# Kernel optimization log

Hardware: AMD Instinct MI355X
Metric: run time of the kernel (lower is better)

Reference implementation:

```python
import jax, jax.numpy as jnp
import numpy as np

DIM = 1024
HEADS = 16
HEAD_DIM = 64
WINDOW = 64


def setup_inputs() -> dict:
    key = jax.random.key(0)
    ks = jax.random.split(key, 9)
    s = lambda fan_in: 1.0 / np.sqrt(fan_in)
    x = jax.random.normal(ks[0], (2, 2048, DIM), dtype=jnp.float32)
    # KANEXLayer: phi = Linear(dim, hidden=dim) -> SiLU -> Linear(dim, dim); g = Linear(dim, 3*H*D)
    W1 = jax.random.uniform(ks[1], (DIM, DIM), jnp.float32, -s(DIM), s(DIM))
    b1 = jax.random.uniform(ks[2], (DIM,), jnp.float32, -s(DIM), s(DIM))
    W2 = jax.random.uniform(ks[3], (DIM, DIM), jnp.float32, -s(DIM), s(DIM))
    b2 = jax.random.uniform(ks[4], (DIM,), jnp.float32, -s(DIM), s(DIM))
    Wg = jax.random.uniform(ks[5], (3 * HEADS * HEAD_DIM, DIM), jnp.float32, -s(DIM), s(DIM))
    bg = jax.random.uniform(ks[6], (3 * HEADS * HEAD_DIM,), jnp.float32, -s(DIM), s(DIM))
    Wo = jax.random.uniform(ks[7], (DIM, HEADS * HEAD_DIM), jnp.float32, -s(HEADS * HEAD_DIM), s(HEADS * HEAD_DIM))
    bo = jax.random.uniform(ks[8], (DIM,), jnp.float32, -s(HEADS * HEAD_DIM), s(HEADS * HEAD_DIM))
    return {"x": x, "W1": W1, "b1": b1, "W2": W2, "b2": b2,
            "Wg": Wg, "bg": bg, "Wo": Wo, "bo": bo}


def reference(x, W1, b1, W2, b2, Wg, bg, Wo, bo):
    b, n, _ = x.shape
    # KANEXLayer: g(phi(x))
    h = jax.nn.silu(x @ W1.T + b1) @ W2.T + b2          # [b, n, dim]
    qkv = h @ Wg.T + bg                                  # [b, n, 3*H*D]
    q, k, v = jnp.split(qkv, 3, axis=-1)
    reshape = lambda t: t.reshape(b, n, HEADS, HEAD_DIM).transpose(0, 2, 1, 3)  # [b, H, n, D]
    q, k, v = reshape(q), reshape(k), reshape(v)
    dots = jnp.einsum('bhid,bhjd->bhij', q, k) * (HEAD_DIM ** -0.5)  # [b, H, n, n]
    # mask positions j >= i + window (triu with diagonal=window_size)
    i = jnp.arange(n)[:, None]
    j = jnp.arange(n)[None, :]
    mask = j >= i + WINDOW                               # [n, n] bool
    dots = jnp.where(mask, -jnp.inf, dots)
    attn = jax.nn.softmax(dots, axis=-1)
    out = jnp.einsum('bhij,bhjd->bhid', attn, v)         # [b, H, n, D]
    out = out.transpose(0, 2, 1, 3).reshape(b, n, HEADS * HEAD_DIM)
    return out @ Wo.T + bo                               # [b, n, dim]
```

## Files before the change

kernel.cpp:

```cpp
#include <hip/hip_runtime.h>

typedef unsigned short u16;
typedef unsigned int   u32;
typedef __bf16 bf16x8 __attribute__((ext_vector_type(8)));
typedef float  f32x4  __attribute__((ext_vector_type(4)));

__device__ __forceinline__ u16 f2bf(float f) {
    return __builtin_bit_cast(u16, (__bf16)f);
}

__device__ __forceinline__ void gload16(const void* g, void* lds) {
    __builtin_amdgcn_global_load_lds(
        (const __attribute__((address_space(1))) u32*)g,
        (__attribute__((address_space(3))) u32*)lds, 16, 0, 0);
}

__device__ __forceinline__ f32x4 mfma16(bf16x8 a, bf16x8 b, f32x4 c) {
    return __builtin_amdgcn_mfma_f32_16x16x32_bf16(a, b, c, 0, 0, 0);
}

__global__ __launch_bounds__(256) void k_cvt5(const float* __restrict__ x,
                                              const float* __restrict__ W1,
                                              const float* __restrict__ W2,
                                              const float* __restrict__ Wg,
                                              const float* __restrict__ Wo,
                                              u16* __restrict__ xb, u16* __restrict__ w1b,
                                              u16* __restrict__ w2b, u16* __restrict__ wgb,
                                              u16* __restrict__ wob) {
    int i = blockIdx.x * 256 + threadIdx.x;
    const float* src; u16* dst; int off;
    if (i < 1048576)      { src = x;  dst = xb;  off = 0; }
    else if (i < 1310720) { src = W1; dst = w1b; off = 1048576; }
    else if (i < 1572864) { src = W2; dst = w2b; off = 1310720; }
    else if (i < 2359296) { src = Wg; dst = wgb; off = 1572864; }
    else                  { src = Wo; dst = wob; off = 2359296; }
    int j = i - off;
    float4 v = ((const float4*)src)[j];
    ushort4 o;
    o.x = f2bf(v.x); o.y = f2bf(v.y); o.z = f2bf(v.z); o.w = f2bf(v.w);
    ((ushort4*)dst)[j] = o;
}

template<bool SILU, bool OUT_BF16, bool VTOUT>
__global__ __launch_bounds__(512) void k_gemm(const u16* __restrict__ A,
                                              const u16* __restrict__ B,
                                              const float* __restrict__ bias,
                                              void* __restrict__ Cout,
                                              int M, int N, int K, int qcols,
                                              u16* __restrict__ vtout) {
    __shared__ __align__(16) u16 As[2][128 * 64];
    __shared__ __align__(16) u16 Bs[2][128 * 64];
    const int tid = threadIdx.x;
    const int w = tid >> 6, l = tid & 63;
    const int wm = w >> 2, wn = w & 3;
    const int lr = l & 15, lg = l >> 4;

    const int nwg = gridDim.x * gridDim.y;
    const int hw = blockIdx.x + gridDim.x * blockIdx.y;
    const int wg = (hw & 7) * (nwg >> 3) + (hw >> 3);
    const int m0 = (wg % gridDim.x) * 128, n0 = (wg / gridDim.x) * 128;

    f32x4 acc[4][2];
#pragma unroll
    for (int i = 0; i < 4; ++i)
#pragma unroll
        for (int j = 0; j < 2; ++j) acc[i][j] = (f32x4){0.f, 0.f, 0.f, 0.f};

    const int srow = l >> 3;
    const int ss = (l & 7) ^ (srow & 7);
    auto STAGE = [&](int buf, int kt) {
#pragma unroll
        for (int i = 0; i < 4; ++i) {
            const int g = w * 4 + i;
            if (g < 16)
                gload16(&A[(size_t)(m0 + g * 8 + srow) * K + kt * 64 + ss * 8],
                        &As[buf][g * 512]);
            else
                gload16(&B[(size_t)(n0 + (g - 16) * 8 + srow) * K + kt * 64 + ss * 8],
                        &Bs[buf][(g - 16) * 512]);
        }
    };

    const int nkt = K >> 6;
    STAGE(0, 0);
    __syncthreads();
    for (int kt = 0; kt < nkt; ++kt) {
        const int cur = kt & 1;
        if (kt + 1 < nkt) STAGE(cur ^ 1, kt + 1);
#pragma unroll
        for (int s = 0; s < 2; ++s) {
            bf16x8 af[4], bq[2];
#pragma unroll
            for (int f = 0; f < 4; ++f) {
                const int r = wm * 64 + f * 16 + lr;
                af[f] = *(const bf16x8*)&As[cur][r * 64 + (((s * 4 + lg) ^ (r & 7)) * 8)];
            }
#pragma unroll
            for (int n = 0; n < 2; ++n) {
                const int r = wn * 32 + n * 16 + lr;
                bq[n] = *(const bf16x8*)&Bs[cur][r * 64 + (((s * 4 + lg) ^ (r & 7)) * 8)];
            }
#pragma unroll
            for (int mf = 0; mf < 4; ++mf)
#pragma unroll
                for (int nf = 0; nf < 2; ++nf)
                    acc[mf][nf] = mfma16(af[mf], bq[nf], acc[mf][nf]);
        }
        if (kt + 1 < nkt) __syncthreads();
    }

#pragma unroll
    for (int nf = 0; nf < 2; ++nf) {
        const int col = n0 + wn * 32 + nf * 16 + lr;
        const float bv = bias[col];
        const float cs = (col < qcols) ? 0.18033688011112042f : 1.0f;
#pragma unroll
        for (int mf = 0; mf < 4; ++mf) {
            float vv[4];
#pragma unroll
            for (int r = 0; r < 4; ++r) {
                float v = acc[mf][nf][r] + bv;
                if (SILU) v = v / (1.0f + __expf(-v));
                vv[r] = v * cs;
            }
            const int row0 = m0 + wm * 64 + mf * 16 + lg * 4;
            if (VTOUT && col >= 2048) {
                const int dfull = col - 2048;
                const int bh = (row0 >> 11) * 16 + (dfull >> 6);
                const int d = dfull & 63;
                const int n = row0 & 2047;
                ushort4 pw;
                pw.x = f2bf(vv[0]); pw.y = f2bf(vv[1]);
                pw.z = f2bf(vv[2]); pw.w = f2bf(vv[3]);
                *(ushort4*)&vtout[(size_t)(bh * 64 + d) * 2048 + n] = pw;
            } else if (OUT_BF16) {
#pragma unroll
                for (int r = 0; r < 4; ++r)
                    ((u16*)Cout)[(size_t)(row0 + r) * N + col] = f2bf(vv[r]);
            } else {
#pragma unroll
                for (int r = 0; r < 4; ++r)
                    ((float*)Cout)[(size_t)(row0 + r) * N + col] = vv[r];
            }
        }
    }
}

__device__ __forceinline__ void attn_leg(const u16* __restrict__ Ksb,
                                         const u16* __restrict__ Vsb,
                                         u16* __restrict__ Plw,
                                         int lr, int lg, bf16x8 q0, bf16x8 q1,
                                         f32x4 (&o)[4], float& ls,
                                         int thr, bool domask) {
    f32x4 st[4];
#pragma unroll
    for (int f = 0; f < 4; ++f) st[f] = (f32x4){0.f, 0.f, 0.f, 0.f};
    __builtin_amdgcn_s_setprio(1);
#pragma unroll
    for (int s = 0; s < 2; ++s) {
        const bf16x8 qf = s ? q1 : q0;
#pragma unroll
        for (int f = 0; f < 4; ++f) {
            const int row = f * 16 + lr;
            const int sw = ((s * 4 + lg) ^ (row & 7)) * 8;
            bf16x8 kf = *(const bf16x8*)&Ksb[row * 64 + sw];
            st[f] = mfma16(kf, qf, st[f]);
        }
    }
    __builtin_amdgcn_s_setprio(0);
    const int kbase = lg * 4;
#pragma unroll
    for (int f = 0; f < 4; ++f) {
        float pv[4];
#pragma unroll
        for (int r = 0; r < 4; ++r) {
            float sv = st[f][r];
            if (domask) sv = (f * 16 + kbase + r > thr) ? -1e30f : sv;
            pv[r] = exp2f(sv);
            ls += pv[r];
        }
        ushort4 pw;
        pw.x = f2bf(pv[0]); pw.y = f2bf(pv[1]); pw.z = f2bf(pv[2]); pw.w = f2bf(pv[3]);
        *(ushort4*)&Plw[lr * 80 + f * 16 + kbase] = pw;
    }
    __builtin_amdgcn_s_setprio(1);
#pragma unroll
    for (int s = 0; s < 2; ++s) {
        const bf16x8 pf = *(const bf16x8*)&Plw[lr * 80 + s * 32 + lg * 8];
#pragma unroll
        for (int f = 0; f < 4; ++f) {
            const int row = f * 16 + lr;
            const int sw = ((s * 4 + lg) ^ (row & 7)) * 8;
            bf16x8 vf = *(const bf16x8*)&Vsb[row * 64 + sw];
            o[f] = mfma16(pf, vf, o[f]);
        }
    }
    __builtin_amdgcn_s_setprio(0);
}

__global__ __launch_bounds__(512) void k_attn(const u16* __restrict__ qkv,
                                              const u16* __restrict__ vt,
                                              u16* __restrict__ ao) {
    __shared__ __align__(16) u16 Ks[2][64 * 64];
    __shared__ __align__(16) u16 Vs[2][64 * 64];
    __shared__ __align__(16) u16 Pl[8][16 * 80];
    const int hw = blockIdx.x + 16 * blockIdx.y;
    const int logical = (hw & 7) * 64 + (hw >> 3);
    const int p = logical & 15, bh = logical >> 4;
    const int b = bh >> 4, h = bh & 15;
    const int tid = threadIdx.x, w = tid >> 6, l = tid & 63;
    const int lr = l & 15, lg = l >> 4;
    const int i = (w >> 2) ? (31 - p) : p;
    const int nt = min(i + 2, 32);
    const int ntL = min(33 - p, 32);

    const size_t qb = (size_t)(b * 2048 + i * 64 + (w & 3) * 16 + lr) * 3072 + h * 64;
    const bf16x8 q0 = *(const bf16x8*)&qkv[qb + lg * 8];
    const bf16x8 q1 = *(const bf16x8*)&qkv[qb + 32 + lg * 8];

    f32x4 o[4];
#pragma unroll
    for (int f = 0; f < 4; ++f) o[f] = (f32x4){0.f, 0.f, 0.f, 0.f};
    float ls = 0.f;
    const int ql = i * 64 + (w & 3) * 16 + lr;

    const int srow = tid >> 3;
    const int ss = (tid & 7) ^ (srow & 7);
    auto STAGE = [&](int buf, int t) {
        const int j0 = t * 64;
        gload16(&qkv[(size_t)(b * 2048 + j0 + srow) * 3072 + 1024 + h * 64 + ss * 8],
                &Ks[buf][tid * 8]);
        gload16(&vt[(size_t)(bh * 64 + srow) * 2048 + j0 + ss * 8], &Vs[buf][tid * 8]);
    };

    STAGE(0, 0);
    __syncthreads();
    for (int t = 0; t < ntL; ++t) {
        const int cur = t & 1;
        if (t + 1 < ntL) STAGE(cur ^ 1, t + 1);
        if (t < nt)
            attn_leg(Ks[cur], Vs[cur], Pl[w], lr, lg, q0, q1, o, ls,
                     ql + 63 - t * 64, t == nt - 1);
        __syncthreads();
    }

    ls += __shfl_xor(ls, 16); ls += __shfl_xor(ls, 32);
    float li[4];
#pragma unroll
    for (int r = 0; r < 4; ++r) li[r] = 1.0f / __shfl(ls, lg * 4 + r);
#pragma unroll
    for (int f = 0; f < 4; ++f) {
#pragma unroll
        for (int r = 0; r < 4; ++r) {
            const int row = b * 2048 + i * 64 + (w & 3) * 16 + lg * 4 + r;
            ao[(size_t)row * 1024 + h * 64 + f * 16 + lr] = f2bf(o[f][r] * li[r]);
        }
    }
}

extern "C" void kernel_launch(void* const* d_in, const int* in_sizes, int n_in,
                              void* d_out, int out_size, void* d_ws, size_t ws_size,
                              hipStream_t stream) {
    const float* x  = (const float*)d_in[0];
    const float* W1 = (const float*)d_in[1];
    const float* b1 = (const float*)d_in[2];
    const float* W2 = (const float*)d_in[3];
    const float* b2 = (const float*)d_in[4];
    const float* Wg = (const float*)d_in[5];
    const float* bg = (const float*)d_in[6];
    const float* Wo = (const float*)d_in[7];
    const float* bo = (const float*)d_in[8];
    float* out = (float*)d_out;

    char* ws = (char*)d_ws;
    const size_t MB = 1024 * 1024;
    u16* x_bf   = (u16*)(ws + 0);
    u16* w1_bf  = (u16*)(ws + 8  * MB);
    u16* w2_bf  = (u16*)(ws + 10 * MB);
    u16* wg_bf  = (u16*)(ws + 12 * MB);
    u16* wo_bf  = (u16*)(ws + 18 * MB);
    u16* h1_bf  = (u16*)(ws + 20 * MB);
    u16* h_bf   = (u16*)(ws + 28 * MB);
    u16* qkv_bf = (u16*)(ws + 36 * MB);
    u16* vt_bf  = (u16*)(ws + 60 * MB);
    u16* ao_bf  = (u16*)(ws + 68 * MB);

    k_cvt5<<<10240, 256, 0, stream>>>(x, W1, W2, Wg, Wo,
                                      x_bf, w1_bf, w2_bf, wg_bf, wo_bf);

    k_gemm<true,  true,  false><<<dim3(32, 8),  512, 0, stream>>>(x_bf,  w1_bf, b1, h1_bf,  4096, 1024, 1024, 0, nullptr);
    k_gemm<false, true,  false><<<dim3(32, 8),  512, 0, stream>>>(h1_bf, w2_bf, b2, h_bf,   4096, 1024, 1024, 0, nullptr);
    k_gemm<false, true,  true ><<<dim3(32, 24), 512, 0, stream>>>(h_bf,  wg_bf, bg, qkv_bf, 4096, 3072, 1024, 1024, vt_bf);

    k_attn<<<dim3(16, 32), 512, 0, stream>>>(qkv_bf, vt_bf, ao_bf);

    k_gemm<false, false, false><<<dim3(32, 8), 512, 0, stream>>>(ao_bf, wo_bf, bo, out, 4096, 1024, 1024, 0, nullptr);
}
```

Before: 157.0 us.

## Stage V-transpose through LDS and pair adjacent query tiles per attention block

The GEMM epilogue for V columns now writes the tile to shared memory with an XOR swizzle and then stores it transposed with 16-byte coalesced writes. This replaces the earlier scattered 8-byte strided stores. The attention kernel now assigns each block two adjacent query tiles (2p, 2p+1) instead of the balanced pair (p, 31-p), and reverses p order across waves to keep some load balance. Adjacent tiles share most K/V tiles, but per-block work becomes uneven, so load balance relies on the block ordering.

After: 161.7 us. +3.0%, slower.

```diff
diff --git a/kernel.cpp b/kernel.cpp
--- a/kernel.cpp
+++ b/kernel.cpp
@@ -109,6 +109,37 @@
         if (kt + 1 < nkt) __syncthreads();
     }
 
+    if (VTOUT && n0 >= 2048) {
+        __syncthreads();
+        u16* tl = &As[0][0];
+#pragma unroll
+        for (int nf = 0; nf < 2; ++nf) {
+            const int cl = wn * 32 + nf * 16 + lr;
+            const float bv = bias[n0 + cl];
+            const int xr = (cl & 7) << 4;
+#pragma unroll
+            for (int mf = 0; mf < 4; ++mf) {
+#pragma unroll
+                for (int r = 0; r < 4; ++r) {
+                    const int ml = wm * 64 + mf * 16 + lg * 4 + r;
+                    tl[cl * 128 + (ml ^ xr)] = f2bf(acc[mf][nf][r] + bv);
+                }
+            }
+        }
+        __syncthreads();
+        const int dl = tid >> 2;
+        const int t0 = (tid & 3) * 32;
+        const int dfull = (n0 - 2048) + dl;
+        const int bhg = (m0 >> 11) * 16 + (dfull >> 6);
+        const size_t vrow = (size_t)(bhg * 64 + (dfull & 63)) * 2048 + (m0 & 2047) + t0;
+        const int xr = (dl & 7) << 4;
+#pragma unroll
+        for (int c = 0; c < 4; ++c) {
+            bf16x8 vv = *(const bf16x8*)&tl[dl * 128 + ((t0 + c * 8) ^ xr)];
+            *(bf16x8*)&vtout[vrow + c * 8] = vv;
+        }
+        return;
+    }
 #pragma unroll
     for (int nf = 0; nf < 2; ++nf) {
         const int col = n0 + wn * 32 + nf * 16 + lr;
@@ -124,16 +155,7 @@
                 vv[r] = v * cs;
             }
             const int row0 = m0 + wm * 64 + mf * 16 + lg * 4;
-            if (VTOUT && col >= 2048) {
-                const int dfull = col - 2048;
-                const int bh = (row0 >> 11) * 16 + (dfull >> 6);
-                const int d = dfull & 63;
-                const int n = row0 & 2047;
-                ushort4 pw;
-                pw.x = f2bf(vv[0]); pw.y = f2bf(vv[1]);
-                pw.z = f2bf(vv[2]); pw.w = f2bf(vv[3]);
-                *(ushort4*)&vtout[(size_t)(bh * 64 + d) * 2048 + n] = pw;
-            } else if (OUT_BF16) {
+            if (OUT_BF16) {
 #pragma unroll
                 for (int r = 0; r < 4; ++r)
                     ((u16*)Cout)[(size_t)(row0 + r) * N + col] = f2bf(vv[r]);
@@ -205,14 +227,16 @@
     __shared__ __align__(16) u16 Vs[2][64 * 64];
     __shared__ __align__(16) u16 Pl[8][16 * 80];
     const int hw = blockIdx.x + 16 * blockIdx.y;
-    const int logical = (hw & 7) * 64 + (hw >> 3);
-    const int p = logical & 15, bh = logical >> 4;
+    const int xcd = hw & 7, u = hw >> 3;
+    const int um = u & 15;
+    const int p = (u < 32) ? um : (15 - um);
+    const int bh = xcd * 4 + (u >> 4);
     const int b = bh >> 4, h = bh & 15;
     const int tid = threadIdx.x, w = tid >> 6, l = tid & 63;
     const int lr = l & 15, lg = l >> 4;
-    const int i = (w >> 2) ? (31 - p) : p;
+    const int i = (w >> 2) ? (2 * p + 1) : (2 * p);
     const int nt = min(i + 2, 32);
-    const int ntL = min(33 - p, 32);
+    const int ntL = min(2 * p + 3, 32);
 
     const size_t qb = (size_t)(b * 2048 + i * 64 + (w & 3) * 16 + lr) * 3072 + h * 64;
     const bf16x8 q0 = *(const bf16x8*)&qkv[qb + lg * 8];
```
